# Performance work log

Measured on AMD Instinct MI355X. Metric: run time of the kernel, lower is better.

## Reference

```python
import jax, jax.numpy as jnp
import numpy as np

N = 50000      # nodes
E = 400000     # edges
NODE_IN = 16
EDGE_IN = 8
H = 4          # heads (layer 1)
C = 64         # hidden_dim
HC = H * C     # 256


def setup_inputs() -> dict:
    key = jax.random.key(0)
    ks = iter(jax.random.split(key, 48))
    def rn(shape, s=0.05):
        return jax.random.normal(next(ks), shape, jnp.float32) * s
    x = jax.random.normal(next(ks), (N, NODE_IN), jnp.float32)
    edge_index = jax.random.randint(next(ks), (2, E), 0, N)
    edge_attr = jax.random.normal(next(ks), (E, EDGE_IN), jnp.float32)
    params = dict(
        # conv1: GATv2Conv(node_in -> hidden, heads=4, concat=True, edge_dim=edge_in)
        Wl1=rn((NODE_IN, HC)), bl1=jnp.zeros((HC,), jnp.float32),
        Wr1=rn((NODE_IN, HC)), br1=jnp.zeros((HC,), jnp.float32),
        We1=rn((EDGE_IN, HC)), att1=rn((H, C)), bias1=jnp.zeros((HC,), jnp.float32),
        # conv2: GATv2Conv(hidden*heads -> hidden, heads=1, concat=False)
        Wl2=rn((HC, C)), bl2=jnp.zeros((C,), jnp.float32),
        Wr2=rn((HC, C)), br2=jnp.zeros((C,), jnp.float32),
        We2=rn((EDGE_IN, C)), att2=rn((1, C)), bias2=jnp.zeros((C,), jnp.float32),
        # batchnorms (eval mode: running stats)
        bn1_g=jnp.ones((HC,), jnp.float32), bn1_b=jnp.zeros((HC,), jnp.float32),
        bn1_m=rn((HC,), 0.01), bn1_v=jnp.ones((HC,), jnp.float32),
        bn2_g=jnp.ones((C,), jnp.float32), bn2_b=jnp.zeros((C,), jnp.float32),
        bn2_m=rn((C,), 0.01), bn2_v=jnp.ones((C,), jnp.float32),
        # residual projection
        Wres=rn((NODE_IN, HC)),
        Wm1=rn((2 * C + EDGE_IN, C)), bm1=jnp.zeros((C,), jnp.float32),
        Wm2=rn((C, C // 2)), bm2=jnp.zeros((C // 2,), jnp.float32),
        Wm3=rn((C // 2, 1)), bm3=jnp.zeros((1,), jnp.float32),
    )
    return dict(x=x, edge_index=edge_index, edge_attr=edge_attr, **params)


def _gatv2(x, src, dst, e_attr, Wl, bl, Wr, br, We, att, bias, heads, out_ch, concat):
    """GATv2Conv message passing (PyG semantics, self-loops already in src/dst)."""
    n = x.shape[0]
    xl = (x @ Wl + bl).reshape(n, heads, out_ch)   # source transform
    xr = (x @ Wr + br).reshape(n, heads, out_ch)   # target transform
    ee = (e_attr @ We).reshape(-1, heads, out_ch)  # edge transform
    # per-edge attention logits: leaky_relu(x_i + x_j + e) . att
    m = jax.nn.leaky_relu(xl[src] + xr[dst] + ee, 0.2)        # [Etot, H, C]
    alpha = jnp.einsum('ehc,hc->eh', m, att)                  # [Etot, H]
    # segment softmax over destination nodes (every node has a self-loop)
    amax = jax.ops.segment_max(alpha, dst, num_segments=n)    # [N, H]
    expa = jnp.exp(alpha - amax[dst])
    denom = jax.ops.segment_sum(expa, dst, num_segments=n)    # [N, H]
    a = expa / (denom[dst] + 1e-16)
    out = jax.ops.segment_sum(xl[src] * a[:, :, None], dst, num_segments=n)  # [N, H, C]
    out = out.reshape(n, heads * out_ch) if concat else out.mean(axis=1)
    return out + bias


def _bn(h, g, b, m, v):
    return (h - m) * jax.lax.rsqrt(v + 1e-5) * g + b


def _forward(x, edge_attr, Wl1, bl1, Wr1, br1, We1, att1, bias1,
             Wl2, bl2, Wr2, br2, We2, att2, bias2,
             bn1_g, bn1_b, bn1_m, bn1_v, bn2_g, bn2_b, bn2_m, bn2_v,
             Wres, Wm1, bm1, Wm2, bm2, Wm3, bm3, edge_index):
    row, col = edge_index[0], edge_index[1]
    # add self-loops with fill_value='mean' for edge_attr (GATv2Conv default)
    loop = jnp.arange(N)
    src = jnp.concatenate([row, loop])
    dst = jnp.concatenate([col, loop])
    ea_mean = edge_attr.mean(axis=0, keepdims=True)
    ea_full = jnp.concatenate([edge_attr, jnp.broadcast_to(ea_mean, (N, EDGE_IN))], axis=0)
    h = _gatv2(x, src, dst, ea_full, Wl1, bl1, Wr1, br1, We1, att1, bias1, H, C, True)
    h = _bn(h, bn1_g, bn1_b, bn1_m, bn1_v)
    h = jax.nn.elu(h + x @ Wres)                 # residual; dropout is a no-op in eval
    h = _gatv2(h, src, dst, ea_full, Wl2, bl2, Wr2, br2, We2, att2, bias2, 1, C, False)
    h = _bn(h, bn2_g, bn2_b, bn2_m, bn2_v)
    h = jax.nn.elu(h)
    # edge head: gather endpoint embeddings + edge_attr -> MLP -> sigmoid
    er = jnp.concatenate([h[row], h[col], edge_attr], axis=-1)   # [E, 2C+edge_in]
    z = jax.nn.gelu(er @ Wm1 + bm1, approximate=False)
    z = jax.nn.gelu(z @ Wm2 + bm2, approximate=False)
    return jax.nn.sigmoid(z @ Wm3 + bm3)[:, 0]                    # [E]


def reference(x, edge_index, edge_attr, Wl1, bl1, Wr1, br1, We1, att1, bias1,
              Wl2, bl2, Wr2, br2, We2, att2, bias2,
              bn1_g, bn1_b, bn1_m, bn1_v, bn2_g, bn2_b, bn2_m, bn2_v,
              Wres, Wm1, bm1, Wm2, bm2, Wm3, bm3):
    return _forward(x, edge_attr, Wl1, bl1, Wr1, br1, We1, att1, bias1,
                    Wl2, bl2, Wr2, br2, We2, att2, bias2,
                    bn1_g, bn1_b, bn1_m, bn1_v, bn2_g, bn2_b, bn2_m, bn2_v,
                    Wres, Wm1, bm1, Wm2, bm2, Wm3, bm3, edge_index)
```

## Files before the change

kernel.cpp:

```cpp
#include <hip/hip_runtime.h>
#include <hip/hip_bf16.h>
#include <hip/hip_fp16.h>
#include <math.h>

#define NN 50000
#define EE 400000
#define ETOT (NN + EE)

__device__ __forceinline__ float gelu_f(float x) {
    return 0.5f * x * (1.f + erff(x * 0.7071067811865476f));
}
__device__ __forceinline__ float elu_f(float x) {
    return x > 0.f ? x : expm1f(x);
}
__device__ __forceinline__ float4 half8_lo_hi(uint4 raw, float4* hi) {
    __half2 h0 = *(__half2*)&raw.x, h1 = *(__half2*)&raw.y;
    __half2 h2 = *(__half2*)&raw.z, h3 = *(__half2*)&raw.w;
    float2 f0 = __half22float2(h0), f1 = __half22float2(h1);
    float2 f2 = __half22float2(h2), f3 = __half22float2(h3);
    *hi = make_float4(f2.x, f2.y, f3.x, f3.y);
    return make_float4(f0.x, f0.y, f1.x, f1.y);
}
__device__ __forceinline__ float4 half4_to_f4(uint2 raw) {
    __half2 a = *(__half2*)&raw.x, b = *(__half2*)&raw.y;
    float2 fa = __half22float2(a), fb = __half22float2(b);
    return make_float4(fa.x, fa.y, fb.x, fb.y);
}
__device__ __forceinline__ uint2 f4_to_half4(float4 v) {
    __half2 h0 = __floats2half2_rn(v.x, v.y);
    __half2 h1 = __floats2half2_rn(v.z, v.w);
    uint2 pk;
    pk.x = *(unsigned*)&h0;
    pk.y = *(unsigned*)&h1;
    return pk;
}
__device__ __forceinline__ uint4 pack8_half(float4 a, float4 b) {
    __half2 q0 = __floats2half2_rn(a.x, a.y), q1 = __floats2half2_rn(a.z, a.w);
    __half2 q2 = __floats2half2_rn(b.x, b.y), q3 = __floats2half2_rn(b.z, b.w);
    uint4 pk;
    pk.x = *(unsigned*)&q0; pk.y = *(unsigned*)&q1;
    pk.z = *(unsigned*)&q2; pk.w = *(unsigned*)&q3;
    return pk;
}
__device__ __forceinline__ void unpack8_half(int x, int y, int z, int w, float* ev) {
    float2 f0 = __half22float2(*(__half2*)&x);
    float2 f1 = __half22float2(*(__half2*)&y);
    float2 f2 = __half22float2(*(__half2*)&z);
    float2 f3 = __half22float2(*(__half2*)&w);
    ev[0] = f0.x; ev[1] = f0.y; ev[2] = f1.x; ev[3] = f1.y;
    ev[4] = f2.x; ev[5] = f2.y; ev[6] = f3.x; ev[7] = f3.y;
}

__global__ __launch_bounds__(256) void k_init(const float* __restrict__ ea, float* __restrict__ ea_sum,
                                              __half* __restrict__ eah,
                                              const int* __restrict__ ei, int* __restrict__ counts,
                                              int E, int N) {
    int t = threadIdx.x;
    if (blockIdx.x < 256) {
        float s[8];
#pragma unroll
        for (int i = 0; i < 8; i++) s[i] = 0.f;
        for (int e = blockIdx.x * 256 + t; e < E; e += 256 * 256) {
            const float4* p = (const float4*)(ea + (size_t)e * 8);
            float4 a = p[0], b = p[1];
            s[0] += a.x; s[1] += a.y; s[2] += a.z; s[3] += a.w;
            s[4] += b.x; s[5] += b.y; s[6] += b.z; s[7] += b.w;
            *(uint4*)(eah + (size_t)e * 8) = pack8_half(a, b);
        }
#pragma unroll
        for (int o = 32; o; o >>= 1)
#pragma unroll
            for (int i = 0; i < 8; i++) s[i] += __shfl_xor(s[i], o, 64);
        __shared__ float sh[4][8];
        int lane = t & 63, w = t >> 6;
        if (lane == 0)
#pragma unroll
            for (int i = 0; i < 8; i++) sh[w][i] = s[i];
        __syncthreads();
        if (t < 8) {
            float v = sh[0][t] + sh[1][t] + sh[2][t] + sh[3][t];
            atomicAdd(ea_sum + t, v);
        }
    } else {
        int e = (blockIdx.x - 256) * 256 + t;
        if (e >= E + N) return;
        int d = (e < E) ? ei[E + e] : (e - E);
        atomicAdd(counts + d, 1);
    }
}

__global__ __launch_bounds__(1024) void k_scan(const int* __restrict__ counts, int* __restrict__ off,
                                               int* __restrict__ cursor, int N) {
    __shared__ int buf[1024];
    int t = threadIdx.x;
    int carry = 0;
    if (t == 0) off[0] = 0;
    for (int base = 0; base < N; base += 4096) {
        int i0 = base + t * 4;
        int v0 = 0, v1 = 0, v2 = 0, v3 = 0;
        if (i0 + 3 < N) {
            int4 vv = *(const int4*)(counts + i0);
            v0 = vv.x; v1 = vv.y; v2 = vv.z; v3 = vv.w;
        } else {
            if (i0 < N)     v0 = counts[i0];
            if (i0 + 1 < N) v1 = counts[i0 + 1];
            if (i0 + 2 < N) v2 = counts[i0 + 2];
            if (i0 + 3 < N) v3 = counts[i0 + 3];
        }
        int s01 = v0 + v1, s012 = s01 + v2, tot4 = s012 + v3;
        buf[t] = tot4;
        __syncthreads();
        for (int o = 1; o < 1024; o <<= 1) {
            int add = (t >= o) ? buf[t - o] : 0;
            __syncthreads();
            buf[t] += add;
            __syncthreads();
        }
        int incl4 = buf[t] + carry;
        int excl = incl4 - tot4;
        if (i0 < N)     { off[i0 + 1] = excl + v0;   cursor[i0]     = excl; }
        if (i0 + 1 < N) { off[i0 + 2] = excl + s01;  cursor[i0 + 1] = excl + v0; }
        if (i0 + 2 < N) { off[i0 + 3] = excl + s012; cursor[i0 + 2] = excl + s01; }
        if (i0 + 3 < N) { off[i0 + 4] = excl + tot4; cursor[i0 + 3] = excl + s012; }
        int tot = buf[1023];
        __syncthreads();
        carry += tot;
    }
}

__global__ __launch_bounds__(256) void k_scat_nt1(const int* __restrict__ ei, int* __restrict__ cursor,
                                                  int* __restrict__ csr_src, int* __restrict__ csr_eid,
                                                  const float* __restrict__ x,
                                                  const float* __restrict__ Wl, const float* __restrict__ bl,
                                                  const float* __restrict__ Wr, const float* __restrict__ br,
                                                  __half* __restrict__ xl1h, __half* __restrict__ xr1h,
                                                  int E, int N) {
    __shared__ float swl[16 * 256];
    __shared__ float swr[16 * 256];
    __shared__ float sx[32 * 16];
    int t = threadIdx.x;
    int S = (E + N + 255) >> 8;
    if ((int)blockIdx.x < S) {
        int e = blockIdx.x * 256 + t;
        if (e >= E + N) return;
        int s, d;
        if (e < E) { s = ei[e]; d = ei[E + e]; }
        else { s = d = e - E; }
        int pos = atomicAdd(cursor + d, 1);
        csr_src[pos] = s;
        csr_eid[pos] = e;
        return;
    }
    int bid = blockIdx.x - S;
#pragma unroll
    for (int k = 0; k < 16; k++) { swl[k * 256 + t] = Wl[k * 256 + t]; swr[k * 256 + t] = Wr[k * 256 + t]; }
    int n0 = bid * 32;
    for (int i = t; i < 32 * 16; i += 256) {
        int n = n0 + (i >> 4);
        sx[i] = (n < N) ? x[(size_t)n * 16 + (i & 15)] : 0.f;
    }
    __syncthreads();
    float bL = bl[t], bR = br[t];
    for (int ni = 0; ni < 32; ni++) {
        int n = n0 + ni;
        if (n >= N) break;
        float al = bL, ar = bR;
#pragma unroll
        for (int k = 0; k < 16; k++) {
            float xv = sx[ni * 16 + k];
            al += xv * swl[k * 256 + t];
            ar += xv * swr[k * 256 + t];
        }
        xl1h[(size_t)n * 256 + t] = __float2half(al);
        xr1h[(size_t)n * 256 + t] = __float2half(ar);
    }
}

__global__ __launch_bounds__(256) void k_fagg1(const __half* __restrict__ xl1h, const __half* __restrict__ xr1h,
                                               const int* __restrict__ off, const int* __restrict__ csr_src,
                                               const int* __restrict__ csr_eid,
                                               const __half* __restrict__ eah, const float* __restrict__ ea_sum,
                                               const float* __restrict__ We1, const float* __restrict__ att1,
                                               const float* __restrict__ bias1,
                                               const float* __restrict__ x, const float* __restrict__ Wres,
                                               const float* __restrict__ g, const float* __restrict__ bb_,
                                               const float* __restrict__ mm_, const float* __restrict__ vv_,
                                               __half* __restrict__ h1h,
                                               int E, int N) {
    int t = threadIdx.x;
    int lane = t & 63, w = t >> 6;
    int node = blockIdx.x * 4 + w;
    if (node >= N) return;
    int c4 = lane * 4;
    float4 we[8];
#pragma unroll
    for (int k = 0; k < 8; k++) we[k] = *(const float4*)(We1 + k * 256 + c4);
    float4 xr4 = half4_to_f4(*(const uint2*)(xr1h + (size_t)node * 256 + c4));
    float4 at4 = *(const float4*)(att1 + c4);
    float invE = 1.f / (float)E;
    float4 eam0, eam1;
    eam0.x = ea_sum[0] * invE; eam0.y = ea_sum[1] * invE;
    eam0.z = ea_sum[2] * invE; eam0.w = ea_sum[3] * invE;
    eam1.x = ea_sum[4] * invE; eam1.y = ea_sum[5] * invE;
    eam1.z = ea_sum[6] * invE; eam1.w = ea_sum[7] * invE;
    uint4 eamp = pack8_half(eam0, eam1);

    int beg = off[node], end = off[node + 1];
    float sumw = 0.f;
    float4 acc = make_float4(0.f, 0.f, 0.f, 0.f);

    int cb = beg;
    while (cb < end) {
        int cnt = end - cb; if (cnt > 64) cnt = 64;
        int sl = 0;
        uint4 pea = eamp;
        if (lane < cnt) {
            sl = csr_src[cb + lane];
            int el = csr_eid[cb + lane];
            if (el < E) pea = *(const uint4*)(eah + (size_t)el * 8);
        }
        float2 r0 = make_float2(0.f, 0.f), r1 = r0, r2 = r0;
        {
            int s0 = __shfl(sl, 0, 64);
            r0 = *(const float2*)(xl1h + (size_t)s0 * 256 + c4);
            if (cnt > 1) { int s1 = __shfl(sl, 1, 64); r1 = *(const float2*)(xl1h + (size_t)s1 * 256 + c4); }
            if (cnt > 2) { int s2 = __shfl(sl, 2, 64); r2 = *(const float2*)(xl1h + (size_t)s2 * 256 + c4); }
        }
        for (int j = 0; j < cnt; j++) {
            float2 cur = r0;
            r0 = r1; r1 = r2;
            if (j + 3 < cnt) {
                int s3 = __shfl(sl, j + 3, 64);
                r2 = *(const float2*)(xl1h + (size_t)s3 * 256 + c4);
            }
            int ex = __shfl((int)pea.x, j, 64);
            int ey = __shfl((int)pea.y, j, 64);
            int ez = __shfl((int)pea.z, j, 64);
            int ew = __shfl((int)pea.w, j, 64);
            float eav[8];
            unpack8_half(ex, ey, ez, ew, eav);
            const __half2* hp = (const __half2*)&cur;
            float2 lo = __half22float2(hp[0]);
            float2 hi = __half22float2(hp[1]);
            float4 xs = make_float4(lo.x, lo.y, hi.x, hi.y);
            float4 ee = make_float4(0.f, 0.f, 0.f, 0.f);
#pragma unroll
            for (int k = 0; k < 8; k++) {
                ee.x += eav[k] * we[k].x; ee.y += eav[k] * we[k].y;
                ee.z += eav[k] * we[k].z; ee.w += eav[k] * we[k].w;
            }
            float4 v;
            v.x = xs.x + xr4.x + ee.x; v.y = xs.y + xr4.y + ee.y;
            v.z = xs.z + xr4.z + ee.z; v.w = xs.w + xr4.w + ee.w;
            v.x = v.x > 0.f ? v.x : 0.2f * v.x;
            v.y = v.y > 0.f ? v.y : 0.2f * v.y;
            v.z = v.z > 0.f ? v.z : 0.2f * v.z;
            v.w = v.w > 0.f ? v.w : 0.2f * v.w;
            float p = v.x * at4.x + v.y * at4.y + v.z * at4.z + v.w * at4.w;
            p += __shfl_xor(p, 1, 64);
            p += __shfl_xor(p, 2, 64);
            p += __shfl_xor(p, 4, 64);
            p += __shfl_xor(p, 8, 64);
            float wgt = expf(p);
            acc.x += wgt * xs.x;
            acc.y += wgt * xs.y;
            acc.z += wgt * xs.z;
            acc.w += wgt * xs.w;
            sumw += wgt;
        }
        cb += cnt;
    }
    float inv = 1.f / (sumw + 1e-16f);
    float4 r = make_float4(0.f, 0.f, 0.f, 0.f);
#pragma unroll
    for (int q = 0; q < 4; q++) {
        float4 xq = *(const float4*)(x + (size_t)node * 16 + q * 4);
        float xa[4] = { xq.x, xq.y, xq.z, xq.w };
#pragma unroll
        for (int kk = 0; kk < 4; kk++) {
            float4 wv = *(const float4*)(Wres + (size_t)(q * 4 + kk) * 256 + c4);
            r.x += xa[kk] * wv.x; r.y += xa[kk] * wv.y;
            r.z += xa[kk] * wv.z; r.w += xa[kk] * wv.w;
        }
    }
    float4 bi = *(const float4*)(bias1 + c4);
    float4 g4 = *(const float4*)(g + c4);
    float4 b4 = *(const float4*)(bb_ + c4);
    float4 m4 = *(const float4*)(mm_ + c4);
    float4 v4 = *(const float4*)(vv_ + c4);
    float4 o;
    o.x = acc.x * inv + bi.x; o.y = acc.y * inv + bi.y;
    o.z = acc.z * inv + bi.z; o.w = acc.w * inv + bi.w;
    o.x = (o.x - m4.x) * rsqrtf(v4.x + 1e-5f) * g4.x + b4.x + r.x;
    o.y = (o.y - m4.y) * rsqrtf(v4.y + 1e-5f) * g4.y + b4.y + r.y;
    o.z = (o.z - m4.z) * rsqrtf(v4.z + 1e-5f) * g4.z + b4.z + r.z;
    o.w = (o.w - m4.w) * rsqrtf(v4.w + 1e-5f) * g4.w + b4.w + r.w;
    o.x = elu_f(o.x); o.y = elu_f(o.y); o.z = elu_f(o.z); o.w = elu_f(o.w);
    *(uint2*)(h1h + (size_t)node * 256 + c4) = f4_to_half4(o);
}

__global__ __launch_bounds__(256) void k_xlr2(const __half* __restrict__ h1h,
                                              const float* __restrict__ Wl2, const float* __restrict__ bl2,
                                              const float* __restrict__ Wr2, const float* __restrict__ br2,
                                              __half* __restrict__ xl2h, __half* __restrict__ xr2h, int N) {
    __shared__ float sh[32][32];
    __shared__ float sw[32][128];
    int t = threadIdx.x;
    int tr = t >> 5, tc = t & 31;
    int n0 = blockIdx.x * 32;
    float acc[4][4];
#pragma unroll
    for (int i = 0; i < 4; i++)
#pragma unroll
        for (int j = 0; j < 4; j++) acc[i][j] = 0.f;
    for (int k0 = 0; k0 < 256; k0 += 32) {
        {
            int n = t >> 3, kk0 = (t & 7) * 4;
            int gn = n0 + n;
            float4 hv = make_float4(0.f, 0.f, 0.f, 0.f);
            if (gn < N) hv = half4_to_f4(*(const uint2*)(h1h + (size_t)gn * 256 + k0 + kk0));
            sh[kk0 + 0][n] = hv.x; sh[kk0 + 1][n] = hv.y; sh[kk0 + 2][n] = hv.z; sh[kk0 + 3][n] = hv.w;
        }
        for (int i = t; i < 32 * 128; i += 256) {
            int kk = i >> 7, c = i & 127;
            sw[kk][c] = (c < 64) ? Wl2[(size_t)(k0 + kk) * 64 + c] : Wr2[(size_t)(k0 + kk) * 64 + (c - 64)];
        }
        __syncthreads();
#pragma unroll
        for (int kk = 0; kk < 32; kk++) {
            float4 hv = *(const float4*)&sh[kk][tr * 4];
            float4 wv = *(const float4*)&sw[kk][tc * 4];
            float hh[4] = { hv.x, hv.y, hv.z, hv.w };
            float wwv[4] = { wv.x, wv.y, wv.z, wv.w };
#pragma unroll
            for (int i = 0; i < 4; i++)
#pragma unroll
                for (int j = 0; j < 4; j++) acc[i][j] += hh[i] * wwv[j];
        }
        __syncthreads();
    }
#pragma unroll
    for (int i = 0; i < 4; i++) {
        int gn = n0 + tr * 4 + i;
        if (gn >= N) continue;
#pragma unroll
        for (int j = 0; j < 4; j++) {
            int c = tc * 4 + j;
            float vv = acc[i][j];
            if (c < 64) xl2h[(size_t)gn * 64 + c] = __float2half(vv + bl2[c]);
            else        xr2h[(size_t)gn * 64 + (c - 64)] = __float2half(vv + br2[c - 64]);
        }
    }
}

__global__ __launch_bounds__(256) void k_fagg2(const __half* __restrict__ xl2h, const __half* __restrict__ xr2h,
                                               const int* __restrict__ off, const int* __restrict__ csr_src,
                                               const int* __restrict__ csr_eid,
                                               const __half* __restrict__ eah, const float* __restrict__ ea_sum,
                                               const float* __restrict__ We2, const float* __restrict__ att2,
                                               const float* __restrict__ bias2,
                                               const float* __restrict__ g, const float* __restrict__ bb_,
                                               const float* __restrict__ mm_, const float* __restrict__ vv_,
                                               __half* __restrict__ h2h,
                                               int E, int N) {
    int t = threadIdx.x;
    int lane = t & 63, w = t >> 6;
    int node = blockIdx.x * 4 + w;
    if (node >= N) return;
    int seg = lane >> 4;
    int c4 = (lane & 15) * 4;
    float4 we[8];
#pragma unroll
    for (int k = 0; k < 8; k++) we[k] = *(const float4*)(We2 + k * 64 + c4);
    float4 xr4 = half4_to_f4(*(const uint2*)(xr2h + (size_t)node * 64 + c4));
    float4 at4 = *(const float4*)(att2 + c4);
    float invE = 1.f / (float)E;
    float4 eam0, eam1;
    eam0.x = ea_sum[0] * invE; eam0.y = ea_sum[1] * invE;
    eam0.z = ea_sum[2] * invE; eam0.w = ea_sum[3] * invE;
    eam1.x = ea_sum[4] * invE; eam1.y = ea_sum[5] * invE;
    eam1.z = ea_sum[6] * invE; eam1.w = ea_sum[7] * invE;
    uint4 eamp = pack8_half(eam0, eam1);

    int beg = off[node], end = off[node + 1];
    float sumw = 0.f;
    float4 acc = make_float4(0.f, 0.f, 0.f, 0.f);

    int cb = beg;
    while (cb < end) {
        int cnt = end - cb; if (cnt > 64) cnt = 64;
        int sl = 0;
        uint4 pea = eamp;
        if (lane < cnt) {
            sl = csr_src[cb + lane];
            int el = csr_eid[cb + lane];
            if (el < E) pea = *(const uint4*)(eah + (size_t)el * 8);
        }
        int nit = (cnt + 3) >> 2;
        float2 r0, r1;
        {
            int s0 = __shfl(sl, seg, 64);
            r0 = *(const float2*)(xl2h + (size_t)s0 * 64 + c4);
            int s1 = __shfl(sl, (seg + 4) & 63, 64);
            r1 = *(const float2*)(xl2h + (size_t)s1 * 64 + c4);
        }
        for (int it = 0; it < nit; ++it) {
            int jj = it * 4 + seg;
            float2 cur = r0;
            r0 = r1;
            {
                int sn = __shfl(sl, (jj + 8) & 63, 64);
                r1 = *(const float2*)(xl2h + (size_t)sn * 64 + c4);
            }
            int ex = __shfl((int)pea.x, jj, 64);
            int ey = __shfl((int)pea.y, jj, 64);
            int ez = __shfl((int)pea.z, jj, 64);
            int ew = __shfl((int)pea.w, jj, 64);
            float eav[8];
            unpack8_half(ex, ey, ez, ew, eav);
            const __half2* hp = (const __half2*)&cur;
            float2 lo = __half22float2(hp[0]);
            float2 hi = __half22float2(hp[1]);
            float4 xs = make_float4(lo.x, lo.y, hi.x, hi.y);
            float4 ee = make_float4(0.f, 0.f, 0.f, 0.f);
#pragma unroll
            for (int k = 0; k < 8; k++) {
                ee.x += eav[k] * we[k].x; ee.y += eav[k] * we[k].y;
                ee.z += eav[k] * we[k].z; ee.w += eav[k] * we[k].w;
            }
            float4 v;
            v.x = xs.x + xr4.x + ee.x; v.y = xs.y + xr4.y + ee.y;
            v.z = xs.z + xr4.z + ee.z; v.w = xs.w + xr4.w + ee.w;
            v.x = v.x > 0.f ? v.x : 0.2f * v.x;
            v.y = v.y > 0.f ? v.y : 0.2f * v.y;
            v.z = v.z > 0.f ? v.z : 0.2f * v.z;
            v.w = v.w > 0.f ? v.w : 0.2f * v.w;
            float p = v.x * at4.x + v.y * at4.y + v.z * at4.z + v.w * at4.w;
            p += __shfl_xor(p, 1, 64);
            p += __shfl_xor(p, 2, 64);
            p += __shfl_xor(p, 4, 64);
            p += __shfl_xor(p, 8, 64);
            bool valid = jj < cnt;
            float wgt = valid ? expf(p) : 0.f;
            acc.x += wgt * xs.x;
            acc.y += wgt * xs.y;
            acc.z += wgt * xs.z;
            acc.w += wgt * xs.w;
            sumw += wgt;
        }
        cb += cnt;
    }
#pragma unroll
    for (int d = 16; d <= 32; d <<= 1) {
        acc.x += __shfl_xor(acc.x, d, 64);
        acc.y += __shfl_xor(acc.y, d, 64);
        acc.z += __shfl_xor(acc.z, d, 64);
        acc.w += __shfl_xor(acc.w, d, 64);
        sumw  += __shfl_xor(sumw, d, 64);
    }
    float inv = 1.f / (sumw + 1e-16f);
    float4 bi = *(const float4*)(bias2 + c4);
    float4 g4 = *(const float4*)(g + c4);
    float4 b4 = *(const float4*)(bb_ + c4);
    float4 m4 = *(const float4*)(mm_ + c4);
    float4 v4 = *(const float4*)(vv_ + c4);
    float4 o;
    o.x = acc.x * inv + bi.x; o.y = acc.y * inv + bi.y;
    o.z = acc.z * inv + bi.z; o.w = acc.w * inv + bi.w;
    o.x = (o.x - m4.x) * rsqrtf(v4.x + 1e-5f) * g4.x + b4.x;
    o.y = (o.y - m4.y) * rsqrtf(v4.y + 1e-5f) * g4.y + b4.y;
    o.z = (o.z - m4.z) * rsqrtf(v4.z + 1e-5f) * g4.z + b4.z;
    o.w = (o.w - m4.w) * rsqrtf(v4.w + 1e-5f) * g4.w + b4.w;
    if (seg == 0) {
        o.x = elu_f(o.x); o.y = elu_f(o.y); o.z = elu_f(o.z); o.w = elu_f(o.w);
        *(uint2*)(h2h + (size_t)node * 64 + c4) = f4_to_half4(o);
    }
}

__global__ __launch_bounds__(256) void k_uv(const __half* __restrict__ h2h, const float* __restrict__ Wm1,
                                            __half* __restrict__ uh, __half* __restrict__ vh, int N) {
    __shared__ float sh[32][32];
    __shared__ float sw[32][128];
    int t = threadIdx.x;
    int tr = t >> 5, tc = t & 31;
    int n0 = blockIdx.x * 32;
    float acc[4][4];
#pragma unroll
    for (int i = 0; i < 4; i++)
#pragma unroll
        for (int j = 0; j < 4; j++) acc[i][j] = 0.f;
    for (int k0 = 0; k0 < 64; k0 += 32) {
        {
            int n = t >> 3, kk0 = (t & 7) * 4;
            int gn = n0 + n;
            float4 hv = make_float4(0.f, 0.f, 0.f, 0.f);
            if (gn < N) hv = half4_to_f4(*(const uint2*)(h2h + (size_t)gn * 64 + k0 + kk0));
            sh[kk0 + 0][n] = hv.x; sh[kk0 + 1][n] = hv.y; sh[kk0 + 2][n] = hv.z; sh[kk0 + 3][n] = hv.w;
        }
        for (int i = t; i < 32 * 128; i += 256) {
            int kk = i >> 7, c = i & 127;
            sw[kk][c] = (c < 64) ? Wm1[(size_t)(k0 + kk) * 64 + c]
                                 : Wm1[(size_t)(64 + k0 + kk) * 64 + (c - 64)];
        }
        __syncthreads();
#pragma unroll
        for (int kk = 0; kk < 32; kk++) {
            float4 hv = *(const float4*)&sh[kk][tr * 4];
            float4 wv = *(const float4*)&sw[kk][tc * 4];
            float hh[4] = { hv.x, hv.y, hv.z, hv.w };
            float wwv[4] = { wv.x, wv.y, wv.z, wv.w };
#pragma unroll
            for (int i = 0; i < 4; i++)
#pragma unroll
                for (int j = 0; j < 4; j++) acc[i][j] += hh[i] * wwv[j];
        }
        __syncthreads();
    }
#pragma unroll
    for (int i = 0; i < 4; i++) {
        int gn = n0 + tr * 4 + i;
        if (gn >= N) continue;
#pragma unroll
        for (int j = 0; j < 4; j++) {
            int c = tc * 4 + j;
            if (c < 64) uh[(size_t)gn * 64 + c] = __float2half(acc[i][j]);
            else        vh[(size_t)gn * 64 + (c - 64)] = __float2half(acc[i][j]);
        }
    }
}

__global__ __launch_bounds__(256) void k_mlp2(const __half* __restrict__ uh, const __half* __restrict__ vh,
                                              const __half* __restrict__ eah, const int* __restrict__ ei,
                                              const float* __restrict__ Wm1, const float* __restrict__ bm1,
                                              const float* __restrict__ Wm2, const float* __restrict__ bm2,
                                              const float* __restrict__ Wm3, const float* __restrict__ bm3,
                                              float* __restrict__ out, int E) {
    __shared__ float sw2[64 * 32];
    __shared__ float sW1e[8 * 64];
    __shared__ float sb1[64];
    __shared__ int sre[64], sce[64];
    __shared__ float z1[64 * 68];
    int t = threadIdx.x;
    for (int i = t; i < 64 * 32; i += 256) sw2[i] = Wm2[i];
    for (int i = t; i < 512; i += 256) sW1e[i] = Wm1[128 * 64 + i];
    if (t < 64) sb1[t] = bm1[t];
    int e0 = blockIdx.x * 64;
    if (t < 64) {
        int e = e0 + t;
        if (e < E) { sre[t] = ei[e]; sce[t] = ei[E + e]; }
        else { sre[t] = 0; sce[t] = 0; }
    }
    __syncthreads();
    for (int i = t; i < 512; i += 256) {
        int el = i >> 3, q = i & 7;
        int r = sre[el], c = sce[el];
        uint4 ru = *(const uint4*)(uh + (size_t)r * 64 + q * 8);
        uint4 rv = *(const uint4*)(vh + (size_t)c * 64 + q * 8);
        uint4 rea = *(const uint4*)(eah + (size_t)(e0 + el) * 8);
        float av[8];
        unpack8_half((int)rea.x, (int)rea.y, (int)rea.z, (int)rea.w, av);
        float wv[8];
#pragma unroll
        for (int j = 0; j < 8; j++) wv[j] = sb1[q * 8 + j];
#pragma unroll
        for (int k = 0; k < 8; k++) {
            float a = av[k];
#pragma unroll
            for (int j = 0; j < 8; j++) wv[j] += a * sW1e[k * 64 + q * 8 + j];
        }
        float4 uhi, vhi;
        float4 ulo = half8_lo_hi(ru, &uhi);
        float4 vlo = half8_lo_hi(rv, &vhi);
        float4 zlo, zhi;
        zlo.x = gelu_f(ulo.x + vlo.x + wv[0]);
        zlo.y = gelu_f(ulo.y + vlo.y + wv[1]);
        zlo.z = gelu_f(ulo.z + vlo.z + wv[2]);
        zlo.w = gelu_f(ulo.w + vlo.w + wv[3]);
        zhi.x = gelu_f(uhi.x + vhi.x + wv[4]);
        zhi.y = gelu_f(uhi.y + vhi.y + wv[5]);
        zhi.z = gelu_f(uhi.z + vhi.z + wv[6]);
        zhi.w = gelu_f(uhi.w + vhi.w + wv[7]);
        *(float4*)(z1 + el * 68 + q * 8)     = zlo;
        *(float4*)(z1 + el * 68 + q * 8 + 4) = zhi;
    }
    __syncthreads();
    int tr = t >> 3;
    int tc = t & 7;
    float b2[4], w3[4];
#pragma unroll
    for (int j = 0; j < 4; j++) { b2[j] = bm2[tc * 4 + j]; w3[j] = Wm3[tc * 4 + j]; }
    float b3 = bm3[0];
    float acc0[4], acc1[4];
#pragma unroll
    for (int j = 0; j < 4; j++) { acc0[j] = 0.f; acc1[j] = 0.f; }
    const float* z0p = z1 + (tr * 2 + 0) * 68;
    const float* z1p = z1 + (tr * 2 + 1) * 68;
#pragma unroll 8
    for (int k = 0; k < 64; k++) {
        float4 wv = *(const float4*)(sw2 + k * 32 + tc * 4);
        float a0 = z0p[k];
        float a1 = z1p[k];
        acc0[0] += a0 * wv.x; acc0[1] += a0 * wv.y; acc0[2] += a0 * wv.z; acc0[3] += a0 * wv.w;
        acc1[0] += a1 * wv.x; acc1[1] += a1 * wv.y; acc1[2] += a1 * wv.z; acc1[3] += a1 * wv.w;
    }
    float p0 = 0.f, p1 = 0.f;
#pragma unroll
    for (int j = 0; j < 4; j++) {
        p0 += gelu_f(acc0[j] + b2[j]) * w3[j];
        p1 += gelu_f(acc1[j] + b2[j]) * w3[j];
    }
    p0 += __shfl_xor(p0, 1, 64); p0 += __shfl_xor(p0, 2, 64); p0 += __shfl_xor(p0, 4, 64);
    p1 += __shfl_xor(p1, 1, 64); p1 += __shfl_xor(p1, 2, 64); p1 += __shfl_xor(p1, 4, 64);
    if (tc == 0) {
        int e = e0 + tr * 2;
        if (e < E)     out[e]     = 1.f / (1.f + expf(-(p0 + b3)));
        if (e + 1 < E) out[e + 1] = 1.f / (1.f + expf(-(p1 + b3)));
    }
}

extern "C" void kernel_launch(void* const* d_in, const int* in_sizes, int n_in,
                              void* d_out, int out_size, void* d_ws, size_t ws_size,
                              hipStream_t stream) {
    const float* x    = (const float*)d_in[0];
    const int*   ei   = (const int*)d_in[1];
    const float* ea   = (const float*)d_in[2];
    const float* Wl1  = (const float*)d_in[3];
    const float* bl1  = (const float*)d_in[4];
    const float* Wr1  = (const float*)d_in[5];
    const float* br1  = (const float*)d_in[6];
    const float* We1  = (const float*)d_in[7];
    const float* att1 = (const float*)d_in[8];
    const float* bias1= (const float*)d_in[9];
    const float* Wl2  = (const float*)d_in[10];
    const float* bl2  = (const float*)d_in[11];
    const float* Wr2  = (const float*)d_in[12];
    const float* br2  = (const float*)d_in[13];
    const float* We2  = (const float*)d_in[14];
    const float* att2 = (const float*)d_in[15];
    const float* bias2= (const float*)d_in[16];
    const float* bn1g = (const float*)d_in[17];
    const float* bn1b = (const float*)d_in[18];
    const float* bn1m = (const float*)d_in[19];
    const float* bn1v = (const float*)d_in[20];
    const float* bn2g = (const float*)d_in[21];
    const float* bn2b = (const float*)d_in[22];
    const float* bn2m = (const float*)d_in[23];
    const float* bn2v = (const float*)d_in[24];
    const float* Wres = (const float*)d_in[25];
    const float* Wm1  = (const float*)d_in[26];
    const float* bm1  = (const float*)d_in[27];
    const float* Wm2  = (const float*)d_in[28];
    const float* bm2  = (const float*)d_in[29];
    const float* Wm3  = (const float*)d_in[30];
    const float* bm3  = (const float*)d_in[31];
    float* out = (float*)d_out;
    float* ws = (float*)d_ws;

    const int N = NN, E = EE, Etot = ETOT;

    float* ea_sum   = ws;
    int*   counts   = (int*)(ws + 16);
    int*   off      = (int*)(ws + 16 + (size_t)N);
    int*   cursor   = (int*)(ws + 32 + (size_t)2 * N);
    int*   csr_src  = (int*)(ws + 32 + (size_t)3 * N);
    int*   csr_eid  = (int*)(ws + 32 + (size_t)3 * N + Etot);
    size_t base     = 32 + (size_t)3 * N + (size_t)2 * Etot;
    __half* xl1h    = (__half*)(ws + base);
    __half* xl2h    = xl1h;
    __half* h2h     = (__half*)(ws + base + (size_t)128 * N);
    __half* xr1h    = (__half*)(ws + base + (size_t)160 * N);
    __half* h1h     = xr1h;
    __half* xr2h    = (__half*)(ws + base + (size_t)288 * N);
    __half* uh      = xr2h;
    __half* vh      = uh + (size_t)64 * N;
    __half* eah     = (__half*)(ws + base + (size_t)352 * N);

    hipMemsetAsync(ea_sum, 0, 16 * sizeof(float), stream);
    hipMemsetAsync(counts, 0, (size_t)N * sizeof(int), stream);

    int S = (Etot + 255) / 256;
    k_init<<<256 + S, 256, 0, stream>>>(ea, ea_sum, eah, ei, counts, E, N);
    k_scan<<<1, 1024, 0, stream>>>(counts, off, cursor, N);
    k_scat_nt1<<<S + (N + 31) / 32, 256, 0, stream>>>(ei, cursor, csr_src, csr_eid,
                                                      x, Wl1, bl1, Wr1, br1, xl1h, xr1h, E, N);
    k_fagg1<<<(N + 3) / 4, 256, 0, stream>>>(xl1h, xr1h, off, csr_src, csr_eid, eah, ea_sum,
                                             We1, att1, bias1, x, Wres,
                                             bn1g, bn1b, bn1m, bn1v, h1h, E, N);
    k_xlr2<<<(N + 31) / 32, 256, 0, stream>>>(h1h, Wl2, bl2, Wr2, br2, xl2h, xr2h, N);
    k_fagg2<<<(N + 3) / 4, 256, 0, stream>>>(xl2h, xr2h, off, csr_src, csr_eid, eah, ea_sum,
                                             We2, att2, bias2,
                                             bn2g, bn2b, bn2m, bn2v, h2h, E, N);
    k_uv<<<(N + 31) / 32, 256, 0, stream>>>(h2h, Wm1, uh, vh, N);
    k_mlp2<<<(E + 63) / 64, 256, 0, stream>>>(uh, vh, eah, ei, Wm1, bm1, Wm2, bm2, Wm3, bm3, out, E);
}
```

Baseline: 452.2 us.

## Sort nodes by in-degree so aggregation warps get balanced work

Builds a degree histogram in the scan kernel and a counting-sort permutation of nodes by in-degree, clamped at 255. The two aggregation kernels then map each wave to a permuted node, so waves in the same block handle nodes of similar degree. This targets divergence and tail imbalance within blocks. In exchange it adds an extra histogram pass, atomics, and an indirection that scatters the per-node reads and writes.

```diff
diff --git a/kernel.cpp b/kernel.cpp
--- a/kernel.cpp
+++ b/kernel.cpp
@@ -90,8 +90,9 @@
 }
 
 __global__ __launch_bounds__(1024) void k_scan(const int* __restrict__ counts, int* __restrict__ off,
-                                               int* __restrict__ cursor, int N) {
+                                               int* __restrict__ cursor, int* __restrict__ dcur, int N) {
     __shared__ int buf[1024];
+    __shared__ int sbin[256];
     int t = threadIdx.x;
     int carry = 0;
     if (t == 0) off[0] = 0;
@@ -126,10 +127,28 @@
         __syncthreads();
         carry += tot;
     }
+    if (t < 256) sbin[t] = 0;
+    __syncthreads();
+    for (int i = t; i < N; i += 1024) {
+        int d = counts[i]; if (d > 255) d = 255;
+        atomicAdd(&sbin[d], 1);
+    }
+    __syncthreads();
+    if (t < 256) buf[t] = sbin[t];
+    __syncthreads();
+    for (int o = 1; o < 256; o <<= 1) {
+        int add = (t >= o && t < 256) ? buf[t - o] : 0;
+        __syncthreads();
+        if (t < 256) buf[t] += add;
+        __syncthreads();
+    }
+    if (t < 256) dcur[t] = buf[t] - sbin[t];
 }
 
 __global__ __launch_bounds__(256) void k_scat_nt1(const int* __restrict__ ei, int* __restrict__ cursor,
                                                   int* __restrict__ csr_src, int* __restrict__ csr_eid,
+                                                  const int* __restrict__ counts, int* __restrict__ dcur,
+                                                  int* __restrict__ perm,
                                                   const float* __restrict__ x,
                                                   const float* __restrict__ Wl, const float* __restrict__ bl,
                                                   const float* __restrict__ Wr, const float* __restrict__ br,
@@ -140,6 +159,7 @@
     __shared__ float sx[32 * 16];
     int t = threadIdx.x;
     int S = (E + N + 255) >> 8;
+    int P = (N + 255) >> 8;
     if ((int)blockIdx.x < S) {
         int e = blockIdx.x * 256 + t;
         if (e >= E + N) return;
@@ -151,7 +171,16 @@
         csr_eid[pos] = e;
         return;
     }
-    int bid = blockIdx.x - S;
+    if ((int)blockIdx.x < S + P) {
+        int n = (blockIdx.x - S) * 256 + t;
+        if (n < N) {
+            int d = counts[n]; if (d > 255) d = 255;
+            int pos = atomicAdd(dcur + d, 1);
+            perm[pos] = n;
+        }
+        return;
+    }
+    int bid = blockIdx.x - S - P;
 #pragma unroll
     for (int k = 0; k < 16; k++) { swl[k * 256 + t] = Wl[k * 256 + t]; swr[k * 256 + t] = Wr[k * 256 + t]; }
     int n0 = bid * 32;
@@ -178,7 +207,7 @@
 
 __global__ __launch_bounds__(256) void k_fagg1(const __half* __restrict__ xl1h, const __half* __restrict__ xr1h,
                                                const int* __restrict__ off, const int* __restrict__ csr_src,
-                                               const int* __restrict__ csr_eid,
+                                               const int* __restrict__ csr_eid, const int* __restrict__ perm,
                                                const __half* __restrict__ eah, const float* __restrict__ ea_sum,
                                                const float* __restrict__ We1, const float* __restrict__ att1,
                                                const float* __restrict__ bias1,
@@ -189,8 +218,9 @@
                                                int E, int N) {
     int t = threadIdx.x;
     int lane = t & 63, w = t >> 6;
-    int node = blockIdx.x * 4 + w;
-    if (node >= N) return;
+    int idx = blockIdx.x * 4 + w;
+    if (idx >= N) return;
+    int node = perm[idx];
     int c4 = lane * 4;
     float4 we[8];
 #pragma unroll
@@ -355,7 +385,7 @@
 
 __global__ __launch_bounds__(256) void k_fagg2(const __half* __restrict__ xl2h, const __half* __restrict__ xr2h,
                                                const int* __restrict__ off, const int* __restrict__ csr_src,
-                                               const int* __restrict__ csr_eid,
+                                               const int* __restrict__ csr_eid, const int* __restrict__ perm,
                                                const __half* __restrict__ eah, const float* __restrict__ ea_sum,
                                                const float* __restrict__ We2, const float* __restrict__ att2,
                                                const float* __restrict__ bias2,
@@ -365,8 +395,9 @@
                                                int E, int N) {
     int t = threadIdx.x;
     int lane = t & 63, w = t >> 6;
-    int node = blockIdx.x * 4 + w;
-    if (node >= N) return;
+    int idx = blockIdx.x * 4 + w;
+    if (idx >= N) return;
+    int node = perm[idx];
     int seg = lane >> 4;
     int c4 = (lane & 15) * 4;
     float4 we[8];
@@ -674,20 +705,24 @@
     __half* uh      = xr2h;
     __half* vh      = uh + (size_t)64 * N;
     __half* eah     = (__half*)(ws + base + (size_t)352 * N);
+    int*   perm     = (int*)(ws + base + (size_t)352 * N + (size_t)4 * E);
+    int*   dcur     = perm + N;
 
     hipMemsetAsync(ea_sum, 0, 16 * sizeof(float), stream);
     hipMemsetAsync(counts, 0, (size_t)N * sizeof(int), stream);
 
     int S = (Etot + 255) / 256;
+    int P = (N + 255) / 256;
     k_init<<<256 + S, 256, 0, stream>>>(ea, ea_sum, eah, ei, counts, E, N);
-    k_scan<<<1, 1024, 0, stream>>>(counts, off, cursor, N);
-    k_scat_nt1<<<S + (N + 31) / 32, 256, 0, stream>>>(ei, cursor, csr_src, csr_eid,
-                                                      x, Wl1, bl1, Wr1, br1, xl1h, xr1h, E, N);
-    k_fagg1<<<(N + 3) / 4, 256, 0, stream>>>(xl1h, xr1h, off, csr_src, csr_eid, eah, ea_sum,
+    k_scan<<<1, 1024, 0, stream>>>(counts, off, cursor, dcur, N);
+    k_scat_nt1<<<S + P + (N + 31) / 32, 256, 0, stream>>>(ei, cursor, csr_src, csr_eid,
+                                                          counts, dcur, perm,
+                                                          x, Wl1, bl1, Wr1, br1, xl1h, xr1h, E, N);
+    k_fagg1<<<(N + 3) / 4, 256, 0, stream>>>(xl1h, xr1h, off, csr_src, csr_eid, perm, eah, ea_sum,
                                              We1, att1, bias1, x, Wres,
                                              bn1g, bn1b, bn1m, bn1v, h1h, E, N);
     k_xlr2<<<(N + 31) / 32, 256, 0, stream>>>(h1h, Wl2, bl2, Wr2, br2, xl2h, xr2h, N);
-    k_fagg2<<<(N + 3) / 4, 256, 0, stream>>>(xl2h, xr2h, off, csr_src, csr_eid, eah, ea_sum,
+    k_fagg2<<<(N + 3) / 4, 256, 0, stream>>>(xl2h, xr2h, off, csr_src, csr_eid, perm, eah, ea_sum,
                                              We2, att2, bias2,
                                              bn2g, bn2b, bn2m, bn2v, h2h, E, N);
     k_uv<<<(N + 31) / 32, 256, 0, stream>>>(h2h, Wm1, uh, vh, N);
```

Result: slower. 623.5 us (+37.9%).
